# Kernel optimization log

Hardware: AMD Instinct MI355X
Metric: run time of the kernel (lower is better)

Reference implementation:

```python
import jax, jax.numpy as jnp
import numpy as np

N, E = 30000, 480000
NFEAT, NHID, H1 = 512, 256, 4


def setup_inputs() -> dict:
    key = jax.random.key(0)
    ks = jax.random.split(key, 16)
    rn = lambda k, shp, sc: jax.random.normal(k, shp, jnp.float32) * sc
    return {
        'x': rn(ks[0], (N, NFEAT), 1.0),
        'edge_index': jax.random.randint(ks[1], (2, E), 0, N),
        # layer 1: in=512, out=256, heads=4, D=64
        'w_kqv1': rn(ks[2], (NFEAT, 3 * NHID), NFEAT ** -0.5),
        'b_kqv1': jnp.zeros((3 * NHID,), jnp.float32),
        'k_rel1': rn(ks[3], (H1, NHID // H1, NHID // H1), (NHID // H1) ** -0.5),
        'v_rel1': rn(ks[4], (H1, NHID // H1, NHID // H1), (NHID // H1) ** -0.5),
        'p_rel1': jnp.ones((H1,), jnp.float32),
        'w_out1': rn(ks[5], (NHID, NHID), NHID ** -0.5),
        'b_out1': jnp.zeros((NHID,), jnp.float32),
        'skip1': jnp.ones((1,), jnp.float32),
        'bn_gamma': jnp.ones((NHID,), jnp.float32),
        'bn_beta': jnp.zeros((NHID,), jnp.float32),
        # layer 2: in=256, out=256, heads=1, D=256
        'w_kqv2': rn(ks[6], (NHID, 3 * NHID), NHID ** -0.5),
        'b_kqv2': jnp.zeros((3 * NHID,), jnp.float32),
        'k_rel2': rn(ks[7], (1, NHID, NHID), NHID ** -0.5),
        'v_rel2': rn(ks[8], (1, NHID, NHID), NHID ** -0.5),
        'p_rel2': jnp.ones((1,), jnp.float32),
        'w_out2': rn(ks[9], (NHID, NHID), NHID ** -0.5),
        'b_out2': jnp.zeros((NHID,), jnp.float32),
        'skip2': jnp.ones((1,), jnp.float32),
    }


def hgt_conv(x, edge_index, w_kqv, b_kqv, k_rel, v_rel, p_rel, w_out, b_out, skip, heads):
    n = x.shape[0]
    out_ch = w_out.shape[0]
    d = out_ch // heads
    kqv = x @ w_kqv + b_kqv                      # [n, 3*out]
    k, q, v = jnp.split(kqv, 3, axis=1)
    k = k.reshape(n, heads, d)
    q = q.reshape(n, heads, d)
    v = v.reshape(n, heads, d)
    # relation-specific per-head transforms of source K/V (single edge type)
    kp = jnp.einsum('nhd,hde->nhe', k, k_rel)
    vp = jnp.einsum('nhd,hde->nhe', v, v_rel)
    src, dst = edge_index[0], edge_index[1]
    # edge-wise attention logits, scaled + relation prior
    alpha = jnp.einsum('ehd,ehd->eh', q[dst], kp[src]) * p_rel / jnp.sqrt(jnp.float32(d))
    # segment softmax over incoming edges of each dst node
    amax = jax.ops.segment_max(alpha, dst, num_segments=n)   # [n, H]
    ex = jnp.exp(alpha - amax[dst])
    denom = jax.ops.segment_sum(ex, dst, num_segments=n) + 1e-16
    a = ex / denom[dst]                                      # [E, H]
    agg = jax.ops.segment_sum(a[:, :, None] * vp[src], dst, num_segments=n)
    out = jax.nn.gelu(agg.reshape(n, out_ch), approximate=False) @ w_out + b_out
    if x.shape[1] == out_ch:  # skip gate only when dims match (PyG HGTConv)
        s = jax.nn.sigmoid(skip)
        out = s * out + (1.0 - s) * x
    return out


def reference(x, edge_index, w_kqv1, b_kqv1, k_rel1, v_rel1, p_rel1, w_out1, b_out1,
              skip1, bn_gamma, bn_beta, w_kqv2, b_kqv2, k_rel2, v_rel2, p_rel2,
              w_out2, b_out2, skip2):
    h = hgt_conv(x, edge_index, w_kqv1, b_kqv1, k_rel1, v_rel1, p_rel1,
                 w_out1, b_out1, skip1, heads=4)
    # BatchNorm1d (training-mode batch stats) + ReLU; dropout is identity (eval)
    mu = h.mean(axis=0)
    var = h.var(axis=0)
    h = (h - mu) / jnp.sqrt(var + 1e-5) * bn_gamma + bn_beta
    h = jax.nn.relu(h)
    out = hgt_conv(h, edge_index, w_kqv2, b_kqv2, k_rel2, v_rel2, p_rel2,
                   w_out2, b_out2, skip2, heads=1)
    return out
```

## Files before the change

kernel.cpp:

```cpp
#include <hip/hip_runtime.h>
#include <math.h>

#define NN 30000
#define NE 480000

typedef _Float16 f16x8 __attribute__((ext_vector_type(8)));
typedef _Float16 f16x4 __attribute__((ext_vector_type(4)));
typedef _Float16 f16x2 __attribute__((ext_vector_type(2)));
typedef float f32x4 __attribute__((ext_vector_type(4)));

#define GLOAD_LDS16(gp, lp)                                        \
    __builtin_amdgcn_global_load_lds(                              \
        (const __attribute__((address_space(1))) void*)(gp),       \
        (__attribute__((address_space(3))) void*)(lp), 16, 0, 0)

__global__ void zero_int_kernel(int* p, int n) {
    int i = blockIdx.x * blockDim.x + threadIdx.x;
    if (i < n) p[i] = 0;
}
__global__ void zero_float_kernel(float* p, int n) {
    int i = blockIdx.x * blockDim.x + threadIdx.x;
    if (i < n) p[i] = 0.0f;
}

__global__ void deg_kernel(const int* __restrict__ dst, int* __restrict__ deg, int e) {
    int i = blockIdx.x * blockDim.x + threadIdx.x;
    if (i < e) atomicAdd(&deg[dst[i]], 1);
}

__global__ __launch_bounds__(1024) void scan_kernel(
    const int* __restrict__ deg, int* __restrict__ row_start,
    int* __restrict__ pos, int n)
{
    __shared__ int smem[1024];
    const int t = threadIdx.x;
    const int base = t * 32;
    int loc[32];
    int s = 0;
#pragma unroll
    for (int g = 0; g < 8; ++g) {
        int idx = base + g * 4;
        int4 d4;
        if (idx + 3 < n) {
            d4 = *(const int4*)(deg + idx);
        } else {
            d4.x = (idx + 0 < n) ? deg[idx + 0] : 0;
            d4.y = (idx + 1 < n) ? deg[idx + 1] : 0;
            d4.z = (idx + 2 < n) ? deg[idx + 2] : 0;
            d4.w = (idx + 3 < n) ? deg[idx + 3] : 0;
        }
        loc[g * 4 + 0] = s; s += d4.x;
        loc[g * 4 + 1] = s; s += d4.y;
        loc[g * 4 + 2] = s; s += d4.z;
        loc[g * 4 + 3] = s; s += d4.w;
    }
    smem[t] = s;
    __syncthreads();
    for (int off = 1; off < 1024; off <<= 1) {
        int tv = 0;
        if (t >= off) tv = smem[t - off];
        __syncthreads();
        smem[t] += tv;
        __syncthreads();
    }
    const int excl = smem[t] - s;
#pragma unroll
    for (int g = 0; g < 32; ++g) {
        int idx = base + g;
        if (idx < n) {
            int r = excl + loc[g];
            row_start[idx] = r;
            pos[idx] = r;
        }
    }
    if (t == 1023) row_start[n] = smem[1023];
}

__global__ void fill_kernel(const int* __restrict__ src, const int* __restrict__ dst,
                            int* __restrict__ pos, int* __restrict__ csr_src, int e) {
    int i = blockIdx.x * blockDim.x + threadIdx.x;
    if (i < e) {
        int p = atomicAdd(&pos[dst[i]], 1);
        csr_src[p] = src[i];
    }
}

__global__ void cvt_f32_f16_kernel(const float* __restrict__ in, _Float16* __restrict__ out, long n8) {
    long i = blockIdx.x * (long)blockDim.x + threadIdx.x;
    if (i >= n8) return;
    float4 a = ((const float4*)in)[2 * i];
    float4 b = ((const float4*)in)[2 * i + 1];
    f16x8 o = {(_Float16)a.x, (_Float16)a.y, (_Float16)a.z, (_Float16)a.w,
               (_Float16)b.x, (_Float16)b.y, (_Float16)b.z, (_Float16)b.w};
    ((f16x8*)out)[i] = o;
}

__global__ void tcvt_kernel(const float* __restrict__ in, _Float16* __restrict__ outT, int K, int N) {
    int n = blockIdx.x * blockDim.x + threadIdx.x;
    int k = blockIdx.y;
    if (n < N) outT[(long)n * K + k] = (_Float16)in[(long)k * N + n];
}

__global__ void foldw1_kernel(const float* __restrict__ W,
                              const float* __restrict__ krel,
                              const float* __restrict__ vrel,
                              _Float16* __restrict__ BT) {
    int k = blockIdx.x * blockDim.x + threadIdx.x;
    int n = blockIdx.y;
    if (k >= 512) return;
    float acc;
    if (n < 256) {
        int h = n >> 6, e = n & 63;
        const float* wr = W + (long)k * 768 + h * 64;
        const float* kr = krel + h * 4096 + e;
        acc = 0.f;
        for (int d = 0; d < 64; ++d) acc += wr[d] * kr[(long)d * 64];
    } else if (n < 512) {
        acc = W[(long)k * 768 + n];
    } else {
        int m = n - 512, h = m >> 6, e = m & 63;
        const float* wr = W + (long)k * 768 + 512 + h * 64;
        const float* vr = vrel + h * 4096 + e;
        acc = 0.f;
        for (int d = 0; d < 64; ++d) acc += wr[d] * vr[(long)d * 64];
    }
    BT[(long)n * 512 + k] = (_Float16)acc;
}

__global__ void foldb1_kernel(const float* __restrict__ b, const float* __restrict__ krel,
                              const float* __restrict__ vrel, float* __restrict__ bf) {
    int n = blockIdx.x * blockDim.x + threadIdx.x;
    if (n >= 768) return;
    float acc;
    if (n < 256) {
        int h = n >> 6, e = n & 63;
        acc = 0.f;
        for (int d = 0; d < 64; ++d) acc += b[h * 64 + d] * krel[h * 4096 + d * 64 + e];
    } else if (n < 512) {
        acc = b[n];
    } else {
        int m = n - 512, h = m >> 6, e = m & 63;
        acc = 0.f;
        for (int d = 0; d < 64; ++d) acc += b[512 + h * 64 + d] * vrel[h * 4096 + d * 64 + e];
    }
    bf[n] = acc;
}

__global__ void foldw2_kernel(const float* __restrict__ W,
                              const float* __restrict__ krel2,
                              const float* __restrict__ vrel2,
                              _Float16* __restrict__ BT) {
    int k = blockIdx.x * blockDim.x + threadIdx.x;
    int n = blockIdx.y;
    if (k >= 256) return;
    float acc;
    if (n < 256) {
        const float* wr = W + (long)k * 768;
        const float* kr = krel2 + n;
        acc = 0.f;
        for (int d = 0; d < 256; ++d) acc += wr[d] * kr[(long)d * 256];
    } else if (n < 512) {
        acc = W[(long)k * 768 + n];
    } else {
        const float* wr = W + (long)k * 768 + 512;
        const float* vr = vrel2 + (n - 512);
        acc = 0.f;
        for (int d = 0; d < 256; ++d) acc += wr[d] * vr[(long)d * 256];
    }
    BT[(long)n * 256 + k] = (_Float16)acc;
}

__global__ void foldb2_kernel(const float* __restrict__ b, const float* __restrict__ krel2,
                              const float* __restrict__ vrel2, float* __restrict__ bf) {
    int n = blockIdx.x * blockDim.x + threadIdx.x;
    if (n >= 768) return;
    float acc;
    if (n < 256) {
        acc = 0.f;
        for (int d = 0; d < 256; ++d) acc += b[d] * krel2[(long)d * 256 + n];
    } else if (n < 512) {
        acc = b[n];
    } else {
        acc = 0.f;
        for (int d = 0; d < 256; ++d) acc += b[512 + d] * vrel2[(long)d * 256 + (n - 512)];
    }
    bf[n] = acc;
}

__global__ __launch_bounds__(256) void mfma_gemm_kernel(
    const _Float16* __restrict__ A, int lda,
    const _Float16* __restrict__ BT,
    float* __restrict__ Cf,
    _Float16* __restrict__ Ch,
    int ldc, int M, int N, int K,
    const float* __restrict__ bias,
    const float* __restrict__ res,
    const float* __restrict__ skip)
{
    __shared__ __align__(16) _Float16 As[128][32];
    __shared__ __align__(16) _Float16 Bs[128][32];
    const int tid = threadIdx.x;
    const int bm = blockIdx.y * 128, bn = blockIdx.x * 128;
    const int wave = tid >> 6, lane = tid & 63;
    const int wr = wave >> 1, wc = wave & 1;
    const int l16 = lane & 15, quad = lane >> 4;

    const int r0 = tid >> 2, kc0 = (tid & 3) * 8;
    const int r1 = r0 + 64;
    int gra0 = bm + r0; if (gra0 >= M) gra0 = M - 1;
    int gra1 = bm + r1; if (gra1 >= M) gra1 = M - 1;
    const _Float16* a0 = A + (long)gra0 * lda + kc0;
    const _Float16* a1 = A + (long)gra1 * lda + kc0;
    const _Float16* b0 = BT + (long)(bn + r0) * K + kc0;
    const _Float16* b1 = BT + (long)(bn + r1) * K + kc0;

    auto ldsA = (__attribute__((address_space(3))) char*)&As[0][0];
    auto ldsB = (__attribute__((address_space(3))) char*)&Bs[0][0];
    const int wb = wave * 1024;

    f32x4 acc[4][4] = {};

    for (int k0 = 0; k0 < K; k0 += 32) {
        GLOAD_LDS16(a0 + k0, ldsA + wb);
        GLOAD_LDS16(a1 + k0, ldsA + 4096 + wb);
        GLOAD_LDS16(b0 + k0, ldsB + wb);
        GLOAD_LDS16(b1 + k0, ldsB + 4096 + wb);
        __syncthreads();
        f16x8 af[4], bf[4];
#pragma unroll
        for (int i = 0; i < 4; ++i)
            af[i] = *(const f16x8*)&As[64 * wr + 16 * i + l16][quad * 8];
#pragma unroll
        for (int j = 0; j < 4; ++j)
            bf[j] = *(const f16x8*)&Bs[64 * wc + 16 * j + l16][quad * 8];
#pragma unroll
        for (int i = 0; i < 4; ++i)
#pragma unroll
            for (int j = 0; j < 4; ++j)
                acc[i][j] = __builtin_amdgcn_mfma_f32_16x16x32_f16(af[i], bf[j], acc[i][j], 0, 0, 0);
        __syncthreads();
    }

    float s = 1.0f, om = 0.0f;
    if (skip) {
        float sv = 1.0f / (1.0f + __expf(-skip[0]));
        s = sv; om = 1.0f - sv;
    }
#pragma unroll
    for (int i = 0; i < 4; ++i) {
        int gr0 = bm + 64 * wr + 16 * i + quad * 4;
#pragma unroll
        for (int j = 0; j < 4; ++j) {
            int gc = bn + 64 * wc + 16 * j + l16;
            float bv = bias ? bias[gc] : 0.0f;
#pragma unroll
            for (int r = 0; r < 4; ++r) {
                int row = gr0 + r;
                if (row >= M) continue;
                float v = acc[i][j][r] + bv;
                if (res) v = s * v + om * res[(long)row * ldc + gc];
                if (Cf) Cf[(long)row * ldc + gc] = v;
                if (Ch) Ch[(long)row * ldc + gc] = (_Float16)v;
            }
        }
    }
}

template <int H>
__global__ __launch_bounds__(256) void attn_f16kv_kernel(
    const _Float16* __restrict__ qbase, int ldq,
    const _Float16* __restrict__ kp, const _Float16* __restrict__ vp, int ldkv,
    const float* __restrict__ p_rel,
    const int* __restrict__ row_start, const int* __restrict__ csr_src,
    _Float16* __restrict__ agg, int n)
{
    constexpr int D = 256 / H;
    constexpr int GL = D / 8;
    int node = blockIdx.x * 8 + (threadIdx.x >> 5);
    int l32 = threadIdx.x & 31;
    if (node >= n) return;
    const int head = l32 / GL;
    const float scale = p_rel[head] * rsqrtf((float)D);
    const int ch = l32 * 8;
    f16x8 qv = *(const f16x8*)(qbase + (long)node * ldq + ch);
    f16x2 qp[4];
#pragma unroll
    for (int j = 0; j < 4; ++j) { qp[j][0] = qv[2 * j]; qp[j][1] = qv[2 * j + 1]; }

    const _Float16* kpc = kp + ch;
    const _Float16* vpc = vp + ch;
    int e0 = row_start[node], e1 = row_start[node + 1];
    float m = -1e30f, lsum = 0.0f;
    float a[8] = {};

    int e = e0;
    for (; e + 1 < e1; e += 2) {
        int s0 = csr_src[e], s1 = csr_src[e + 1];
        f16x8 k0 = *(const f16x8*)(kpc + (long)s0 * ldkv);
        f16x8 k1 = *(const f16x8*)(kpc + (long)s1 * ldkv);
        f16x8 v0 = *(const f16x8*)(vpc + (long)s0 * ldkv);
        f16x8 v1 = *(const f16x8*)(vpc + (long)s1 * ldkv);
        float d0 = 0.0f, d1 = 0.0f;
#pragma unroll
        for (int j = 0; j < 4; ++j) {
            f16x2 k0p = {k0[2 * j], k0[2 * j + 1]};
            f16x2 k1p = {k1[2 * j], k1[2 * j + 1]};
            d0 = __builtin_amdgcn_fdot2(qp[j], k0p, d0, false);
            d1 = __builtin_amdgcn_fdot2(qp[j], k1p, d1, false);
        }
#pragma unroll
        for (int off = 1; off < GL; off <<= 1) {
            d0 += __shfl_xor(d0, off);
            d1 += __shfl_xor(d1, off);
        }
        float al0 = d0 * scale, al1 = d1 * scale;
        float mx = fmaxf(al0, al1);
        float diff = mx - m;
        if (__builtin_expect(diff > 8.0f, 0)) {
            float corr = __expf(-diff);
            lsum *= corr;
#pragma unroll
            for (int j = 0; j < 8; ++j) a[j] *= corr;
            m = mx;
        }
        float w0 = __expf(al0 - m), w1 = __expf(al1 - m);
        lsum += w0 + w1;
#pragma unroll
        for (int j = 0; j < 8; ++j)
            a[j] += w0 * (float)v0[j] + w1 * (float)v1[j];
    }
    if (e < e1) {
        int s0 = csr_src[e];
        f16x8 k0 = *(const f16x8*)(kpc + (long)s0 * ldkv);
        f16x8 v0 = *(const f16x8*)(vpc + (long)s0 * ldkv);
        float d0 = 0.0f;
#pragma unroll
        for (int j = 0; j < 4; ++j) {
            f16x2 k0p = {k0[2 * j], k0[2 * j + 1]};
            d0 = __builtin_amdgcn_fdot2(qp[j], k0p, d0, false);
        }
#pragma unroll
        for (int off = 1; off < GL; off <<= 1) d0 += __shfl_xor(d0, off);
        float al0 = d0 * scale;
        float diff = al0 - m;
        if (__builtin_expect(diff > 8.0f, 0)) {
            float corr = __expf(-diff);
            lsum *= corr;
#pragma unroll
            for (int j = 0; j < 8; ++j) a[j] *= corr;
            m = al0;
        }
        float w0 = __expf(al0 - m);
        lsum += w0;
#pragma unroll
        for (int j = 0; j < 8; ++j) a[j] += w0 * (float)v0[j];
    }

    float inv = 1.0f / (lsum + 1e-16f);
    f16x8 o;
#pragma unroll
    for (int j = 0; j < 8; ++j) {
        float v = a[j] * inv;
        v = 0.5f * v * (1.0f + erff(v * 0.70710678118654752f));
        o[j] = (_Float16)v;
    }
    *(f16x8*)(agg + (long)node * 256 + ch) = o;
}

__global__ void bn_stats_kernel(const float* __restrict__ h, float* __restrict__ sums,
                                float* __restrict__ sqs, int n) {
    int c = threadIdx.x;
    float s = 0.f, q = 0.f;
    for (int r = blockIdx.x; r < n; r += gridDim.x) {
        float v = h[(long)r * 256 + c];
        s += v;
        q += v * v;
    }
    atomicAdd(&sums[c], s);
    atomicAdd(&sqs[c], q);
}

__global__ void bn_apply_kernel(float* __restrict__ h, _Float16* __restrict__ oh,
                                const float* __restrict__ sums, const float* __restrict__ sqs,
                                const float* __restrict__ gamma, const float* __restrict__ beta) {
    long idx = blockIdx.x * (long)blockDim.x + threadIdx.x;
    if (idx >= (long)NN * 64) return;
    int cg = (int)(idx & 63) * 4;
    float4 hv = ((float4*)h)[idx];
    float vv[4] = {hv.x, hv.y, hv.z, hv.w};
    const float invn = 1.0f / 30000.0f;
    f16x4 ovh;
#pragma unroll
    for (int r = 0; r < 4; ++r) {
        int c = cg + r;
        float mu = sums[c] * invn;
        float var = sqs[c] * invn - mu * mu;
        float v = (vv[r] - mu) * rsqrtf(var + 1e-5f) * gamma[c] + beta[c];
        v = fmaxf(v, 0.0f);
        vv[r] = v;
        ovh[r] = (_Float16)v;
    }
    ((float4*)h)[idx] = make_float4(vv[0], vv[1], vv[2], vv[3]);
    ((f16x4*)oh)[idx] = ovh;
}

extern "C" void kernel_launch(void* const* d_in, const int* in_sizes, int n_in,
                              void* d_out, int out_size, void* d_ws, size_t ws_size,
                              hipStream_t stream) {
    const float* x       = (const float*)d_in[0];
    const int*   ei      = (const int*)d_in[1];
    const float* w_kqv1  = (const float*)d_in[2];
    const float* b_kqv1  = (const float*)d_in[3];
    const float* k_rel1  = (const float*)d_in[4];
    const float* v_rel1  = (const float*)d_in[5];
    const float* p_rel1  = (const float*)d_in[6];
    const float* w_out1  = (const float*)d_in[7];
    const float* b_out1  = (const float*)d_in[8];
    const float* bn_gamma = (const float*)d_in[10];
    const float* bn_beta  = (const float*)d_in[11];
    const float* w_kqv2  = (const float*)d_in[12];
    const float* b_kqv2  = (const float*)d_in[13];
    const float* k_rel2  = (const float*)d_in[14];
    const float* v_rel2  = (const float*)d_in[15];
    const float* p_rel2  = (const float*)d_in[16];
    const float* w_out2  = (const float*)d_in[17];
    const float* b_out2  = (const float*)d_in[18];
    const float* skip2   = (const float*)d_in[19];
    float* out = (float*)d_out;

    char* p = (char*)d_ws;
    auto alloc = [&](size_t bytes) -> void* {
        void* r = (void*)p;
        p += (bytes + 255) & ~(size_t)255;
        return r;
    };
    _Float16* x_h   = (_Float16*)alloc((size_t)NN * 512 * 2);
    _Float16* kqv_h = (_Float16*)alloc((size_t)NN * 768 * 2);
    _Float16* agg_h = (_Float16*)alloc((size_t)NN * 256 * 2);
    float* h     = (float*)alloc((size_t)NN * 256 * 4);
    _Float16* hbn_h = (_Float16*)alloc((size_t)NN * 256 * 2);
    _Float16* w1T    = (_Float16*)alloc((size_t)768 * 512 * 2);
    _Float16* wout1T = (_Float16*)alloc((size_t)256 * 256 * 2);
    _Float16* w2T    = (_Float16*)alloc((size_t)768 * 256 * 2);
    _Float16* wout2T = (_Float16*)alloc((size_t)256 * 256 * 2);
    float* bf1       = (float*)alloc(768 * 4);
    float* bf2       = (float*)alloc(768 * 4);
    int*   deg       = (int*)alloc((size_t)NN * 4);
    int*   row_start = (int*)alloc((size_t)(NN + 1) * 4);
    int*   pos       = (int*)alloc((size_t)NN * 4);
    int*   csr_src   = (int*)alloc((size_t)NE * 4);
    float* bnsum     = (float*)alloc(256 * 4);
    float* bnsq      = (float*)alloc(256 * 4);

    const int* esrc = ei;
    const int* edst = ei + NE;

    cvt_f32_f16_kernel<<<(NN * 512 / 8 + 255) / 256, 256, 0, stream>>>(x, x_h, (long)NN * 512 / 8);
    foldw1_kernel<<<dim3(2, 768), 256, 0, stream>>>(w_kqv1, k_rel1, v_rel1, w1T);
    foldb1_kernel<<<3, 256, 0, stream>>>(b_kqv1, k_rel1, v_rel1, bf1);
    tcvt_kernel<<<dim3(1, 256), 256, 0, stream>>>(w_out1, wout1T, 256, 256);
    foldw2_kernel<<<dim3(1, 768), 256, 0, stream>>>(w_kqv2, k_rel2, v_rel2, w2T);
    foldb2_kernel<<<3, 256, 0, stream>>>(b_kqv2, k_rel2, v_rel2, bf2);
    tcvt_kernel<<<dim3(1, 256), 256, 0, stream>>>(w_out2, wout2T, 256, 256);

    zero_int_kernel<<<(NN + 255) / 256, 256, 0, stream>>>(deg, NN);
    deg_kernel<<<(NE + 255) / 256, 256, 0, stream>>>(edst, deg, NE);
    scan_kernel<<<1, 1024, 0, stream>>>(deg, row_start, pos, NN);
    fill_kernel<<<(NE + 255) / 256, 256, 0, stream>>>(esrc, edst, pos, csr_src, NE);

    const int MB = (NN + 127) / 128;

    mfma_gemm_kernel<<<dim3(6, MB), 256, 0, stream>>>(
        x_h, 512, w1T, nullptr, kqv_h, 768, NN, 768, 512, bf1, nullptr, nullptr);
    attn_f16kv_kernel<4><<<(NN + 7) / 8, 256, 0, stream>>>(
        kqv_h + 256, 768, kqv_h, kqv_h + 512, 768, p_rel1, row_start, csr_src, agg_h, NN);
    mfma_gemm_kernel<<<dim3(2, MB), 256, 0, stream>>>(
        agg_h, 256, wout1T, h, nullptr, 256, NN, 256, 256, b_out1, nullptr, nullptr);

    zero_float_kernel<<<1, 256, 0, stream>>>(bnsum, 256);
    zero_float_kernel<<<1, 256, 0, stream>>>(bnsq, 256);
    bn_stats_kernel<<<256, 256, 0, stream>>>(h, bnsum, bnsq, NN);
    bn_apply_kernel<<<(NN * 64 + 255) / 256, 256, 0, stream>>>(h, hbn_h, bnsum, bnsq, bn_gamma, bn_beta);

    mfma_gemm_kernel<<<dim3(6, MB), 256, 0, stream>>>(
        hbn_h, 256, w2T, nullptr, kqv_h, 768, NN, 768, 256, bf2, nullptr, nullptr);
    attn_f16kv_kernel<1><<<(NN + 7) / 8, 256, 0, stream>>>(
        kqv_h + 256, 768, kqv_h, kqv_h + 512, 768, p_rel2, row_start, csr_src, agg_h, NN);
    mfma_gemm_kernel<<<dim3(2, MB), 256, 0, stream>>>(
        agg_h, 256, wout2T, out, nullptr, 256, NN, 256, 256, b_out2, h, skip2);
}
```

Before: 636.8 us.

## Fuse BatchNorm statistics into GEMM epilogue and unroll attention edge gathers

The output-projection GEMM of layer 1 now accumulates per-column sum and sum-of-squares in its epilogue. These are reduced through shared memory and added atomically, which removes the separate bn_stats pass over h. The intermediate h is stored in fp16, so bn_apply reads and writes half as many bytes, and the layer-2 residual reads the fp16 BN output. The attention kernel loads 16 CSR indices per lane group at once, broadcasts them with shuffles, and processes 4 edges per iteration to keep more gathers in flight. The costs are extra atomics, higher register pressure, and some fp16 rounding of h before normalization.

```diff
diff --git a/kernel.cpp b/kernel.cpp
--- a/kernel.cpp
+++ b/kernel.cpp
@@ -194,8 +194,9 @@
     _Float16* __restrict__ Ch,
     int ldc, int M, int N, int K,
     const float* __restrict__ bias,
-    const float* __restrict__ res,
-    const float* __restrict__ skip)
+    const _Float16* __restrict__ res,
+    const float* __restrict__ skip,
+    float* __restrict__ bn_accum)
 {
     __shared__ __align__(16) _Float16 As[128][32];
     __shared__ __align__(16) _Float16 Bs[128][32];
@@ -246,6 +247,7 @@
         float sv = 1.0f / (1.0f + __expf(-skip[0]));
         s = sv; om = 1.0f - sv;
     }
+    float cs[4] = {}, cq[4] = {};
 #pragma unroll
     for (int i = 0; i < 4; ++i) {
         int gr0 = bm + 64 * wr + 16 * i + quad * 4;
@@ -258,10 +260,33 @@
                 int row = gr0 + r;
                 if (row >= M) continue;
                 float v = acc[i][j][r] + bv;
-                if (res) v = s * v + om * res[(long)row * ldc + gc];
+                if (res) v = s * v + om * (float)res[(long)row * ldc + gc];
                 if (Cf) Cf[(long)row * ldc + gc] = v;
                 if (Ch) Ch[(long)row * ldc + gc] = (_Float16)v;
-            }
+                if (bn_accum) { cs[j] += v; cq[j] += v * v; }
+            }
+        }
+    }
+    if (bn_accum) {
+        float* redS = (float*)&As[0][0];
+        float* redQ = (float*)&Bs[0][0];
+        int slot = wr * 4 + quad;
+#pragma unroll
+        for (int j = 0; j < 4; ++j) {
+            int cl = 64 * wc + 16 * j + l16;
+            redS[cl * 8 + slot] = cs[j];
+            redQ[cl * 8 + slot] = cq[j];
+        }
+        __syncthreads();
+        if (tid < 128) {
+            float ssum = 0.f, qsum = 0.f;
+#pragma unroll
+            for (int t = 0; t < 8; ++t) {
+                ssum += redS[tid * 8 + t];
+                qsum += redQ[tid * 8 + t];
+            }
+            atomicAdd(&bn_accum[bn + tid], ssum);
+            atomicAdd(&bn_accum[256 + bn + tid], qsum);
         }
     }
 }
@@ -293,67 +318,89 @@
     float m = -1e30f, lsum = 0.0f;
     float a[8] = {};
 
-    int e = e0;
-    for (; e + 1 < e1; e += 2) {
-        int s0 = csr_src[e], s1 = csr_src[e + 1];
-        f16x8 k0 = *(const f16x8*)(kpc + (long)s0 * ldkv);
-        f16x8 k1 = *(const f16x8*)(kpc + (long)s1 * ldkv);
-        f16x8 v0 = *(const f16x8*)(vpc + (long)s0 * ldkv);
-        f16x8 v1 = *(const f16x8*)(vpc + (long)s1 * ldkv);
-        float d0 = 0.0f, d1 = 0.0f;
-#pragma unroll
-        for (int j = 0; j < 4; ++j) {
-            f16x2 k0p = {k0[2 * j], k0[2 * j + 1]};
-            f16x2 k1p = {k1[2 * j], k1[2 * j + 1]};
-            d0 = __builtin_amdgcn_fdot2(qp[j], k0p, d0, false);
-            d1 = __builtin_amdgcn_fdot2(qp[j], k1p, d1, false);
-        }
-#pragma unroll
-        for (int off = 1; off < GL; off <<= 1) {
-            d0 += __shfl_xor(d0, off);
-            d1 += __shfl_xor(d1, off);
-        }
-        float al0 = d0 * scale, al1 = d1 * scale;
-        float mx = fmaxf(al0, al1);
-        float diff = mx - m;
-        if (__builtin_expect(diff > 8.0f, 0)) {
-            float corr = __expf(-diff);
-            lsum *= corr;
-#pragma unroll
-            for (int j = 0; j < 8; ++j) a[j] *= corr;
-            m = mx;
-        }
-        float w0 = __expf(al0 - m), w1 = __expf(al1 - m);
-        lsum += w0 + w1;
-#pragma unroll
-        for (int j = 0; j < 8; ++j)
-            a[j] += w0 * (float)v0[j] + w1 * (float)v1[j];
-    }
-    if (e < e1) {
-        int s0 = csr_src[e];
-        f16x8 k0 = *(const f16x8*)(kpc + (long)s0 * ldkv);
-        f16x8 v0 = *(const f16x8*)(vpc + (long)s0 * ldkv);
-        float d0 = 0.0f;
-#pragma unroll
-        for (int j = 0; j < 4; ++j) {
-            f16x2 k0p = {k0[2 * j], k0[2 * j + 1]};
-            d0 = __builtin_amdgcn_fdot2(qp[j], k0p, d0, false);
-        }
-#pragma unroll
-        for (int off = 1; off < GL; off <<= 1) d0 += __shfl_xor(d0, off);
-        float al0 = d0 * scale;
-        float diff = al0 - m;
-        if (__builtin_expect(diff > 8.0f, 0)) {
-            float corr = __expf(-diff);
-            lsum *= corr;
-#pragma unroll
-            for (int j = 0; j < 8; ++j) a[j] *= corr;
-            m = al0;
-        }
-        float w0 = __expf(al0 - m);
-        lsum += w0;
-#pragma unroll
-        for (int j = 0; j < 8; ++j) a[j] += w0 * (float)v0[j];
+    for (int ebase = e0; ebase < e1; ebase += 16) {
+        int cnt = e1 - ebase; if (cnt > 16) cnt = 16;
+        int ip = ebase + (l32 & 15);
+        if (ip > e1 - 1) ip = e1 - 1;
+        int idxreg = csr_src[ip];
+        int i = 0;
+        for (; i + 4 <= cnt; i += 4) {
+            int s0 = __shfl(idxreg, i, 32);
+            int s1 = __shfl(idxreg, i + 1, 32);
+            int s2 = __shfl(idxreg, i + 2, 32);
+            int s3 = __shfl(idxreg, i + 3, 32);
+            f16x8 k0 = *(const f16x8*)(kpc + (long)s0 * ldkv);
+            f16x8 k1 = *(const f16x8*)(kpc + (long)s1 * ldkv);
+            f16x8 k2 = *(const f16x8*)(kpc + (long)s2 * ldkv);
+            f16x8 k3 = *(const f16x8*)(kpc + (long)s3 * ldkv);
+            f16x8 v0 = *(const f16x8*)(vpc + (long)s0 * ldkv);
+            f16x8 v1 = *(const f16x8*)(vpc + (long)s1 * ldkv);
+            f16x8 v2 = *(const f16x8*)(vpc + (long)s2 * ldkv);
+            f16x8 v3 = *(const f16x8*)(vpc + (long)s3 * ldkv);
+            float d0 = 0.f, d1 = 0.f, d2 = 0.f, d3 = 0.f;
+#pragma unroll
+            for (int j = 0; j < 4; ++j) {
+                f16x2 t0 = {k0[2 * j], k0[2 * j + 1]};
+                f16x2 t1 = {k1[2 * j], k1[2 * j + 1]};
+                f16x2 t2 = {k2[2 * j], k2[2 * j + 1]};
+                f16x2 t3 = {k3[2 * j], k3[2 * j + 1]};
+                d0 = __builtin_amdgcn_fdot2(qp[j], t0, d0, false);
+                d1 = __builtin_amdgcn_fdot2(qp[j], t1, d1, false);
+                d2 = __builtin_amdgcn_fdot2(qp[j], t2, d2, false);
+                d3 = __builtin_amdgcn_fdot2(qp[j], t3, d3, false);
+            }
+#pragma unroll
+            for (int off = 1; off < GL; off <<= 1) {
+                d0 += __shfl_xor(d0, off);
+                d1 += __shfl_xor(d1, off);
+                d2 += __shfl_xor(d2, off);
+                d3 += __shfl_xor(d3, off);
+            }
+            float al0 = d0 * scale, al1 = d1 * scale;
+            float al2 = d2 * scale, al3 = d3 * scale;
+            float mx = fmaxf(fmaxf(al0, al1), fmaxf(al2, al3));
+            float diff = mx - m;
+            if (__builtin_expect(diff > 8.0f, 0)) {
+                float corr = __expf(-diff);
+                lsum *= corr;
+#pragma unroll
+                for (int j = 0; j < 8; ++j) a[j] *= corr;
+                m = mx;
+            }
+            float w0 = __expf(al0 - m), w1 = __expf(al1 - m);
+            float w2 = __expf(al2 - m), w3 = __expf(al3 - m);
+            lsum += (w0 + w1) + (w2 + w3);
+#pragma unroll
+            for (int j = 0; j < 8; ++j)
+                a[j] += (w0 * (float)v0[j] + w1 * (float)v1[j]) +
+                        (w2 * (float)v2[j] + w3 * (float)v3[j]);
+        }
+        for (; i < cnt; ++i) {
+            int s0 = __shfl(idxreg, i, 32);
+            f16x8 k0 = *(const f16x8*)(kpc + (long)s0 * ldkv);
+            f16x8 v0 = *(const f16x8*)(vpc + (long)s0 * ldkv);
+            float d0 = 0.f;
+#pragma unroll
+            for (int j = 0; j < 4; ++j) {
+                f16x2 t0 = {k0[2 * j], k0[2 * j + 1]};
+                d0 = __builtin_amdgcn_fdot2(qp[j], t0, d0, false);
+            }
+#pragma unroll
+            for (int off = 1; off < GL; off <<= 1) d0 += __shfl_xor(d0, off);
+            float al0 = d0 * scale;
+            float diff = al0 - m;
+            if (__builtin_expect(diff > 8.0f, 0)) {
+                float corr = __expf(-diff);
+                lsum *= corr;
+#pragma unroll
+                for (int j = 0; j < 8; ++j) a[j] *= corr;
+                m = al0;
+            }
+            float w0 = __expf(al0 - m);
+            lsum += w0;
+#pragma unroll
+            for (int j = 0; j < 8; ++j) a[j] += w0 * (float)v0[j];
+        }
     }
 
     float inv = 1.0f / (lsum + 1e-16f);
@@ -367,41 +414,24 @@
     *(f16x8*)(agg + (long)node * 256 + ch) = o;
 }
 
-__global__ void bn_stats_kernel(const float* __restrict__ h, float* __restrict__ sums,
-                                float* __restrict__ sqs, int n) {
-    int c = threadIdx.x;
-    float s = 0.f, q = 0.f;
-    for (int r = blockIdx.x; r < n; r += gridDim.x) {
-        float v = h[(long)r * 256 + c];
-        s += v;
-        q += v * v;
-    }
-    atomicAdd(&sums[c], s);
-    atomicAdd(&sqs[c], q);
-}
-
-__global__ void bn_apply_kernel(float* __restrict__ h, _Float16* __restrict__ oh,
-                                const float* __restrict__ sums, const float* __restrict__ sqs,
+__global__ void bn_apply_kernel(const _Float16* __restrict__ hin, _Float16* __restrict__ hbn,
+                                const float* __restrict__ stats,
                                 const float* __restrict__ gamma, const float* __restrict__ beta) {
     long idx = blockIdx.x * (long)blockDim.x + threadIdx.x;
-    if (idx >= (long)NN * 64) return;
-    int cg = (int)(idx & 63) * 4;
-    float4 hv = ((float4*)h)[idx];
-    float vv[4] = {hv.x, hv.y, hv.z, hv.w};
+    if (idx >= (long)NN * 32) return;
+    int cg = (int)(idx & 31) * 8;
+    f16x8 hv = ((const f16x8*)hin)[idx];
     const float invn = 1.0f / 30000.0f;
-    f16x4 ovh;
-#pragma unroll
-    for (int r = 0; r < 4; ++r) {
+    f16x8 o;
+#pragma unroll
+    for (int r = 0; r < 8; ++r) {
         int c = cg + r;
-        float mu = sums[c] * invn;
-        float var = sqs[c] * invn - mu * mu;
-        float v = (vv[r] - mu) * rsqrtf(var + 1e-5f) * gamma[c] + beta[c];
-        v = fmaxf(v, 0.0f);
-        vv[r] = v;
-        ovh[r] = (_Float16)v;
-    }
-    ((float4*)h)[idx] = make_float4(vv[0], vv[1], vv[2], vv[3]);
-    ((f16x4*)oh)[idx] = ovh;
+        float mu = stats[c] * invn;
+        float var = stats[256 + c] * invn - mu * mu;
+        float v = ((float)hv[r] - mu) * rsqrtf(var + 1e-5f) * gamma[c] + beta[c];
+        o[r] = (_Float16)fmaxf(v, 0.0f);
+    }
+    ((f16x8*)hbn)[idx] = o;
 }
 
 extern "C" void kernel_launch(void* const* d_in, const int* in_sizes, int n_in,
@@ -437,7 +467,7 @@
     _Float16* x_h   = (_Float16*)alloc((size_t)NN * 512 * 2);
     _Float16* kqv_h = (_Float16*)alloc((size_t)NN * 768 * 2);
     _Float16* agg_h = (_Float16*)alloc((size_t)NN * 256 * 2);
-    float* h     = (float*)alloc((size_t)NN * 256 * 4);
+    _Float16* h16   = (_Float16*)alloc((size_t)NN * 256 * 2);
     _Float16* hbn_h = (_Float16*)alloc((size_t)NN * 256 * 2);
     _Float16* w1T    = (_Float16*)alloc((size_t)768 * 512 * 2);
     _Float16* wout1T = (_Float16*)alloc((size_t)256 * 256 * 2);
@@ -449,8 +479,7 @@
     int*   row_start = (int*)alloc((size_t)(NN + 1) * 4);
     int*   pos       = (int*)alloc((size_t)NN * 4);
     int*   csr_src   = (int*)alloc((size_t)NE * 4);
-    float* bnsum     = (float*)alloc(256 * 4);
-    float* bnsq      = (float*)alloc(256 * 4);
+    float* bnstats   = (float*)alloc(512 * 4);
 
     const int* esrc = ei;
     const int* edst = ei + NE;
@@ -471,21 +500,20 @@
     const int MB = (NN + 127) / 128;
 
     mfma_gemm_kernel<<<dim3(6, MB), 256, 0, stream>>>(
-        x_h, 512, w1T, nullptr, kqv_h, 768, NN, 768, 512, bf1, nullptr, nullptr);
+        x_h, 512, w1T, nullptr, kqv_h, 768, NN, 768, 512, bf1, nullptr, nullptr, nullptr);
     attn_f16kv_kernel<4><<<(NN + 7) / 8, 256, 0, stream>>>(
         kqv_h + 256, 768, kqv_h, kqv_h + 512, 768, p_rel1, row_start, csr_src, agg_h, NN);
+
+    zero_float_kernel<<<2, 256, 0, stream>>>(bnstats, 512);
     mfma_gemm_kernel<<<dim3(2, MB), 256, 0, stream>>>(
-        agg_h, 256, wout1T, h, nullptr, 256, NN, 256, 256, b_out1, nullptr, nullptr);
-
-    zero_float_kernel<<<1, 256, 0, stream>>>(bnsum, 256);
-    zero_float_kernel<<<1, 256, 0, stream>>>(bnsq, 256);
-    bn_stats_kernel<<<256, 256, 0, stream>>>(h, bnsum, bnsq, NN);
-    bn_apply_kernel<<<(NN * 64 + 255) / 256, 256, 0, stream>>>(h, hbn_h, bnsum, bnsq, bn_gamma, bn_beta);
+        agg_h, 256, wout1T, nullptr, h16, 256, NN, 256, 256, b_out1, nullptr, nullptr, bnstats);
+
+    bn_apply_kernel<<<(NN * 32 + 255) / 256, 256, 0, stream>>>(h16, hbn_h, bnstats, bn_gamma, bn_beta);
 
     mfma_gemm_kernel<<<dim3(6, MB), 256, 0, stream>>>(
-        hbn_h, 256, w2T, nullptr, kqv_h, 768, NN, 768, 256, bf2, nullptr, nullptr);
+        hbn_h, 256, w2T, nullptr, kqv_h, 768, NN, 768, 256, bf2, nullptr, nullptr, nullptr);
     attn_f16kv_kernel<1><<<(NN + 7) / 8, 256, 0, stream>>>(
         kqv_h + 256, 768, kqv_h, kqv_h + 512, 768, p_rel2, row_start, csr_src, agg_h, NN);
     mfma_gemm_kernel<<<dim3(2, MB), 256, 0, stream>>>(
-        agg_h, 256, wout2T, out, nullptr, 256, NN, 256, 256, b_out2, h, skip2);
-}
+        agg_h, 256, wout2T, out, nullptr, 256, NN, 256, 256, b_out2, hbn_h, skip2, nullptr);
+}
```

New measurement: 583.9 us. -8.3%, faster.
